# Kernel optimization log

Measured on AMD Instinct MI355X. Metric: run time of the kernel, lower is better.

Reference implementation:

```python
import jax, jax.numpy as jnp
import numpy as np

B = 4
S = 2_000_000
NPIX = 196608  # 12 * 128**2 (HEALPix nside=128)


def setup_inputs() -> dict:
    key = jax.random.key(0)
    k1, k2, k3, k4 = jax.random.split(key, 4)
    tod = jax.random.normal(k1, (B, S), dtype=jnp.float32)
    # per-sample Stokes weights (I, Q, U) of the pointing matrix rows
    weights = jax.random.normal(k2, (S, 3), dtype=jnp.float32)
    projection_cov = jax.random.uniform(k3, (NPIX,), dtype=jnp.float32)
    pix_idx = jax.random.randint(k4, (S,), 0, NPIX, dtype=jnp.int32)
    return {"tod": tod, "weights": weights, "projection_cov": projection_cov,
            "pix_idx": pix_idx}


def reference(tod, weights, projection_cov, pix_idx):
    npix = projection_cov.shape[0]
    # P^T: scatter-add each TOD sample's Stokes contribution into its pixel.
    # contrib: [B, S, 3]
    contrib = tod[:, :, None] * weights[None, :, :]
    sky = jax.vmap(
        lambda c: jax.ops.segment_sum(c, pix_idx, num_segments=npix)
    )(contrib)  # [B, npix, 3]
    # coverage normalization of I, Q, U
    sky = sky / projection_cov[None, :, None]
    return sky
```

## Files before the change

### kernel.cpp

```cpp
#include <hip/hip_runtime.h>


constexpr int NB   = 256;
constexpr int BW   = 768;
constexpr int NBLK = 256;
constexpr int TILE = 2048;
constexpr int RT   = 3072;


__device__ __forceinline__ unsigned f2bf(float f) {
    unsigned u = __float_as_uint(f);
    unsigned r = ((u >> 16) & 1u) + 0x7fffu;
    return (u + r) >> 16;
}
__device__ __forceinline__ float bf_lo(unsigned u) {
    return __uint_as_float(u << 16);
}
__device__ __forceinline__ float bf_hi(unsigned u) {
    return __uint_as_float(u & 0xffff0000u);
}


__global__ __launch_bounds__(1024)
void hist_kernel(const int* __restrict__ pix, int S, int chunk,
                 int* __restrict__ hist2d) {
    __shared__ int lh[NB];
    if (threadIdx.x < NB) lh[threadIdx.x] = 0;
    __syncthreads();
    const int beg = blockIdx.x * chunk;
    const int end = min(S, beg + chunk);
    for (int j = beg + threadIdx.x; j < end; j += blockDim.x)
        atomicAdd(&lh[pix[j] / BW], 1);
    __syncthreads();
    if (threadIdx.x < NB)
        hist2d[(size_t)blockIdx.x * NB + threadIdx.x] = lh[threadIdx.x];
}

__global__ __launch_bounds__(NBLK)
void scan_blocks_kernel(int* __restrict__ hist2d,
                        int* __restrict__ btotal) {
    __shared__ int sc[NBLK];
    const int bkt = blockIdx.x, tid = threadIdx.x;
    const int v = hist2d[(size_t)tid * NB + bkt];
    sc[tid] = v;
    __syncthreads();
    for (int off = 1; off < NBLK; off <<= 1) {
        int x = (tid >= off) ? sc[tid - off] : 0;
        __syncthreads();
        sc[tid] += x;
        __syncthreads();
    }
    hist2d[(size_t)tid * NB + bkt] = sc[tid] - v;
    if (tid == NBLK - 1) btotal[bkt] = sc[tid];
}

__global__ __launch_bounds__(NB)
void scan_buckets_kernel(const int* __restrict__ btotal,
                         int* __restrict__ bbase, int S) {
    __shared__ int sc[NB];
    const int tid = threadIdx.x;
    const int v = btotal[tid];
    sc[tid] = v;
    __syncthreads();
    for (int off = 1; off < NB; off <<= 1) {
        int x = (tid >= off) ? sc[tid - off] : 0;
        __syncthreads();
        sc[tid] += x;
        __syncthreads();
    }
    bbase[tid] = sc[tid] - v;
    if (tid == NB - 1) bbase[NB] = sc[tid];
}

__global__ __launch_bounds__(1024)
void reorder_sorted_kernel(const float* __restrict__ tod,
                           const float* __restrict__ weights,
                           const int* __restrict__ pix,
                           int S, int chunk,
                           const int* __restrict__ hist2d,
                           const int* __restrict__ bbase,
                           uint4* __restrict__ rec) {
    __shared__ unsigned       lrx[RT], lry[RT], lrz[RT], lrw[RT];
    __shared__ unsigned short lbk[RT];
    __shared__ unsigned short lidx[RT];
    __shared__ int            lbase[NB];
    __shared__ int            lcur[NB];
    __shared__ int            lstart[NB];

    const int blk = blockIdx.x;
    if (threadIdx.x < NB) {
        lbase[threadIdx.x] = bbase[threadIdx.x]
                           + hist2d[(size_t)blk * NB + threadIdx.x];
    }
    const int cbeg = blk * chunk;
    const int cend = min(S, cbeg + chunk);
    __syncthreads();

    for (int tbeg = cbeg; tbeg < cend; tbeg += RT) {
        const int n = min(RT, cend - tbeg);

        if (threadIdx.x < NB) lcur[threadIdx.x] = 0;
        __syncthreads();

        for (int jj = threadIdx.x; jj < n; jj += blockDim.x) {
            const int j = tbeg + jj;
            const int p = pix[j];
            const int bkt = p / BW;
            const int lp  = p - bkt * BW;
            const float w0 = weights[3 * j + 0];
            const float w1 = weights[3 * j + 1];
            const float w2 = weights[3 * j + 2];
            const float t0 = tod[(size_t)0 * S + j];
            const float t1 = tod[(size_t)1 * S + j];
            const float t2 = tod[(size_t)2 * S + j];
            const float t3 = tod[(size_t)3 * S + j];
            lrx[jj] = f2bf(w0) | (f2bf(w1) << 16);
            lry[jj] = f2bf(w2) | ((unsigned)lp << 16);
            lrz[jj] = f2bf(t0) | (f2bf(t1) << 16);
            lrw[jj] = f2bf(t2) | (f2bf(t3) << 16);
            lbk[jj] = (unsigned short)bkt;
            atomicAdd(&lcur[bkt], 1);
        }
        __syncthreads();

        if (threadIdx.x < 64) {
            const int i0 = threadIdx.x * 4;
            const int a0 = lcur[i0], a1 = lcur[i0 + 1];
            const int a2 = lcur[i0 + 2], a3 = lcur[i0 + 3];
            const int t1 = a0 + a1, t2 = t1 + a2, t3 = t2 + a3;
            int x = t3;
            #pragma unroll
            for (int off = 1; off < 64; off <<= 1) {
                const int y = __shfl_up(x, off, 64);
                if ((int)threadIdx.x >= off) x += y;
            }
            const int base = x - t3;
            lstart[i0]     = base;
            lstart[i0 + 1] = base + a0;
            lstart[i0 + 2] = base + t1;
            lstart[i0 + 3] = base + t2;
            lcur[i0]     = base;
            lcur[i0 + 1] = base + a0;
            lcur[i0 + 2] = base + t1;
            lcur[i0 + 3] = base + t2;
        }
        __syncthreads();

        for (int jj = threadIdx.x; jj < n; jj += blockDim.x) {
            const int r = atomicAdd(&lcur[lbk[jj]], 1);
            lidx[r] = (unsigned short)jj;
        }
        __syncthreads();

        for (int r = threadIdx.x; r < n; r += blockDim.x) {
            const int jj  = lidx[r];
            const int bkt = lbk[jj];
            uint4 v;
            v.x = lrx[jj]; v.y = lry[jj]; v.z = lrz[jj]; v.w = lrw[jj];
            rec[(size_t)(lbase[bkt] + (r - lstart[bkt]))] = v;
        }
        __syncthreads();

        if (threadIdx.x < NB)
            lbase[threadIdx.x] += lcur[threadIdx.x] - lstart[threadIdx.x];
        __syncthreads();
    }
}

__global__ __launch_bounds__(1024)
void accum_sort_kernel(const uint4* __restrict__ rec,
                       const float* __restrict__ cov,
                       const int* __restrict__ bbase,
                       float* __restrict__ out,
                       int npix) {
    __shared__ uint4          lrec[TILE];
    __shared__ unsigned short lpx[TILE];
    __shared__ unsigned short lidx[TILE];
    __shared__ int            start[BW + 1];
    __shared__ int            cur[BW];

    const int bkt = blockIdx.x;
    const int beg = bbase[bkt], end = bbase[bkt + 1];
    const int l = threadIdx.x & 255;
    const int q = threadIdx.x >> 8;
    float s00 = 0.f, s01 = 0.f, s02 = 0.f;
    float s10 = 0.f, s11 = 0.f, s12 = 0.f;
    float s20 = 0.f, s21 = 0.f, s22 = 0.f;

    for (int tbeg = beg; tbeg < end; tbeg += TILE) {
        const int n = min(TILE, end - tbeg);

        for (int t = threadIdx.x; t < BW; t += blockDim.x) cur[t] = 0;
        __syncthreads();
        for (int j = threadIdx.x; j < n; j += blockDim.x) {
            const uint4 r = rec[(size_t)(tbeg + j)];
            lrec[j] = r;
            const int lp = (int)(r.y >> 16);
            lpx[j] = (unsigned short)lp;
            atomicAdd(&cur[lp], 1);
        }
        __syncthreads();

        if (threadIdx.x < 64) {
            const int i0 = threadIdx.x * 12;
            int v[12], pre[12], run = 0;
            #pragma unroll
            for (int k = 0; k < 12; ++k) {
                v[k] = cur[i0 + k]; pre[k] = run; run += v[k];
            }
            int x = run;
            #pragma unroll
            for (int off = 1; off < 64; off <<= 1) {
                const int y = __shfl_up(x, off, 64);
                if ((int)threadIdx.x >= off) x += y;
            }
            const int base = x - run;
            #pragma unroll
            for (int k = 0; k < 12; ++k) {
                start[i0 + k] = base + pre[k];
                cur[i0 + k]   = base + pre[k];
            }
            if (threadIdx.x == 63) start[BW] = base + run;
        }
        __syncthreads();

        for (int j = threadIdx.x; j < n; j += blockDim.x) {
            const int r = atomicAdd(&cur[lpx[j]], 1);
            lidx[r] = (unsigned short)j;
        }
        __syncthreads();

        {
            const int rb = start[l], re = start[l + 1];
            for (int j = rb; j < re; ++j) {
                const int i = lidx[j];
                const uint4 r = lrec[i];
                const float tq = (q == 0) ? bf_lo(r.z) : (q == 1) ? bf_hi(r.z)
                               : (q == 2) ? bf_lo(r.w) : bf_hi(r.w);
                s00 += tq * bf_lo(r.x);
                s01 += tq * bf_hi(r.x);
                s02 += tq * bf_lo(r.y);
            }
        }
        {
            const int rb = start[l + 256], re = start[l + 257];
            for (int j = rb; j < re; ++j) {
                const int i = lidx[j];
                const uint4 r = lrec[i];
                const float tq = (q == 0) ? bf_lo(r.z) : (q == 1) ? bf_hi(r.z)
                               : (q == 2) ? bf_lo(r.w) : bf_hi(r.w);
                s10 += tq * bf_lo(r.x);
                s11 += tq * bf_hi(r.x);
                s12 += tq * bf_lo(r.y);
            }
        }
        {
            const int rb = start[l + 512], re = start[l + 513];
            for (int j = rb; j < re; ++j) {
                const int i = lidx[j];
                const uint4 r = lrec[i];
                const float tq = (q == 0) ? bf_lo(r.z) : (q == 1) ? bf_hi(r.z)
                               : (q == 2) ? bf_lo(r.w) : bf_hi(r.w);
                s20 += tq * bf_lo(r.x);
                s21 += tq * bf_hi(r.x);
                s22 += tq * bf_lo(r.y);
            }
        }
        __syncthreads();
    }

    {
        const int p = bkt * BW + l;
        const float rc = 1.0f / cov[p];
        const size_t o = ((size_t)q * npix + p) * 3;
        out[o + 0] = s00 * rc; out[o + 1] = s01 * rc; out[o + 2] = s02 * rc;
    }
    {
        const int p = bkt * BW + 256 + l;
        const float rc = 1.0f / cov[p];
        const size_t o = ((size_t)q * npix + p) * 3;
        out[o + 0] = s10 * rc; out[o + 1] = s11 * rc; out[o + 2] = s12 * rc;
    }
    {
        const int p = bkt * BW + 512 + l;
        const float rc = 1.0f / cov[p];
        const size_t o = ((size_t)q * npix + p) * 3;
        out[o + 0] = s20 * rc; out[o + 1] = s21 * rc; out[o + 2] = s22 * rc;
    }
}


__global__ void zero_out_kernel(float4* __restrict__ out, int n4) {
    int i = blockIdx.x * blockDim.x + threadIdx.x;
    int stride = gridDim.x * blockDim.x;
    for (; i < n4; i += stride) out[i] = make_float4(0.f, 0.f, 0.f, 0.f);
}

__global__ void scatter_kernel(const float* __restrict__ tod,
                               const float* __restrict__ weights,
                               const int*   __restrict__ pix,
                               float* __restrict__ out,
                               int S, int npix, int B) {
    int i = blockIdx.x * blockDim.x + threadIdx.x;
    int stride = gridDim.x * blockDim.x;
    const size_t bstride = (size_t)npix * 3;
    for (int s = i; s < S; s += stride) {
        const int p = pix[s];
        const float w0 = weights[3 * s + 0];
        const float w1 = weights[3 * s + 1];
        const float w2 = weights[3 * s + 2];
        float* o = out + (size_t)p * 3;
        for (int b = 0; b < B; ++b) {
            const float t = tod[(size_t)b * S + s];
            float* ob = o + (size_t)b * bstride;
            atomicAdd(ob + 0, t * w0);
            atomicAdd(ob + 1, t * w1);
            atomicAdd(ob + 2, t * w2);
        }
    }
}

__global__ void normalize_kernel(float* __restrict__ out,
                                 const float* __restrict__ cov,
                                 int npix, int B) {
    int i = blockIdx.x * blockDim.x + threadIdx.x;
    int stride = gridDim.x * blockDim.x;
    const int total = B * npix;
    for (; i < total; i += stride) {
        const int p = i % npix;
        const float c = cov[p];
        float* o = out + (size_t)i * 3;
        o[0] /= c; o[1] /= c; o[2] /= c;
    }
}


extern "C" void kernel_launch(void* const* d_in, const int* in_sizes, int n_in,
                              void* d_out, int out_size, void* d_ws, size_t ws_size,
                              hipStream_t stream) {
    const float* tod     = (const float*)d_in[0];
    const float* weights = (const float*)d_in[1];
    const float* cov     = (const float*)d_in[2];
    const int*   pix     = (const int*)d_in[3];
    float* out = (float*)d_out;

    const int S    = in_sizes[3];
    const int npix = in_sizes[2];
    const int B    = in_sizes[0] / S;

    const size_t meta_ints  = (size_t)NB * NBLK + NB + (NB + 1);
    const size_t meta_bytes = ((meta_ints * sizeof(int)) + 63) & ~(size_t)63;
    const size_t need_rec   = meta_bytes + (size_t)S * 16;

    const int chunk = (S + NBLK - 1) / NBLK;

    if (B == 4 && npix == NB * BW && ws_size >= need_rec) {
        int* hist2d = (int*)d_ws;
        int* btotal = hist2d + (size_t)NB * NBLK;
        int* bbase  = btotal + NB;
        uint4* rec  = (uint4*)((char*)d_ws + meta_bytes);

        hist_kernel<<<NBLK, 1024, 0, stream>>>(pix, S, chunk, hist2d);
        scan_blocks_kernel<<<NB, NBLK, 0, stream>>>(hist2d, btotal);
        scan_buckets_kernel<<<1, NB, 0, stream>>>(btotal, bbase, S);
        reorder_sorted_kernel<<<NBLK, 1024, 0, stream>>>(tod, weights, pix, S,
                                                         chunk, hist2d, bbase, rec);
        accum_sort_kernel<<<NB, 1024, 0, stream>>>(rec, cov, bbase, out, npix);
        return;
    }

    const int block = 256;
    {
        const int n4 = out_size / 4;
        int grid = min((n4 + block - 1) / block, 2048);
        zero_out_kernel<<<grid, block, 0, stream>>>((float4*)out, n4);
    }
    {
        int grid = min((S + block - 1) / block, 4096);
        scatter_kernel<<<grid, block, 0, stream>>>(tod, weights, pix, out, S, npix, B);
    }
    {
        const int total = B * npix;
        int grid = min((total + block - 1) / block, 2048);
        normalize_kernel<<<grid, block, 0, stream>>>(out, cov, npix, B);
    }
}
```

Baseline: 71.08 us.

## Split per-bucket accumulation across two blocks and add a reduce-normalize pass

Each pixel bucket's record range is now split into PARTS=2 halves, each handled by its own block, so the accumulation grid doubles from 256 to 512 blocks to fill more compute units. Each block writes unnormalized partial sums to a workspace buffer, and a new kernel adds the partials and applies the coverage normalization. The shared record tile also moves from uint4 to four separate unsigned arrays (structure-of-arrays) to change the LDS access pattern. In exchange it adds a kernel launch and extra global traffic to write and reread the partial sums, and it needs a larger workspace.

```diff
diff --git a/kernel.cpp b/kernel.cpp
--- a/kernel.cpp
+++ b/kernel.cpp
@@ -1,11 +1,12 @@
 #include <hip/hip_runtime.h>
 
 
-constexpr int NB   = 256;
-constexpr int BW   = 768;
-constexpr int NBLK = 256;
-constexpr int TILE = 2048;
-constexpr int RT   = 3072;
+constexpr int NB    = 256;
+constexpr int BW    = 768;
+constexpr int NBLK  = 256;
+constexpr int TILE  = 2048;
+constexpr int RT    = 3072;
+constexpr int PARTS = 2;
 
 
 __device__ __forceinline__ unsigned f2bf(float f) {
@@ -168,19 +169,24 @@
 }
 
 __global__ __launch_bounds__(1024)
-void accum_sort_kernel(const uint4* __restrict__ rec,
-                       const float* __restrict__ cov,
+void accum_part_kernel(const uint4* __restrict__ rec,
                        const int* __restrict__ bbase,
-                       float* __restrict__ out,
+                       float* __restrict__ partial,
                        int npix) {
-    __shared__ uint4          lrec[TILE];
+    __shared__ unsigned       lrx[TILE], lry[TILE], lrz[TILE], lrw[TILE];
     __shared__ unsigned short lpx[TILE];
     __shared__ unsigned short lidx[TILE];
     __shared__ int            start[BW + 1];
     __shared__ int            cur[BW];
 
-    const int bkt = blockIdx.x;
-    const int beg = bbase[bkt], end = bbase[bkt + 1];
+    const int bkt  = blockIdx.x / PARTS;
+    const int part = blockIdx.x - bkt * PARTS;
+    const int bbeg = bbase[bkt], bend = bbase[bkt + 1];
+    const int len  = bend - bbeg;
+    const int cl   = (len + PARTS - 1) / PARTS;
+    const int beg  = bbeg + part * cl;
+    const int end  = min(bend, beg + cl);
+
     const int l = threadIdx.x & 255;
     const int q = threadIdx.x >> 8;
     float s00 = 0.f, s01 = 0.f, s02 = 0.f;
@@ -194,7 +200,7 @@
         __syncthreads();
         for (int j = threadIdx.x; j < n; j += blockDim.x) {
             const uint4 r = rec[(size_t)(tbeg + j)];
-            lrec[j] = r;
+            lrx[j] = r.x; lry[j] = r.y; lrz[j] = r.z; lrw[j] = r.w;
             const int lp = (int)(r.y >> 16);
             lpx[j] = (unsigned short)lp;
             atomicAdd(&cur[lp], 1);
@@ -234,58 +240,79 @@
             const int rb = start[l], re = start[l + 1];
             for (int j = rb; j < re; ++j) {
                 const int i = lidx[j];
-                const uint4 r = lrec[i];
-                const float tq = (q == 0) ? bf_lo(r.z) : (q == 1) ? bf_hi(r.z)
-                               : (q == 2) ? bf_lo(r.w) : bf_hi(r.w);
-                s00 += tq * bf_lo(r.x);
-                s01 += tq * bf_hi(r.x);
-                s02 += tq * bf_lo(r.y);
+                const float tq = (q == 0) ? bf_lo(lrz[i]) : (q == 1) ? bf_hi(lrz[i])
+                               : (q == 2) ? bf_lo(lrw[i]) : bf_hi(lrw[i]);
+                s00 += tq * bf_lo(lrx[i]);
+                s01 += tq * bf_hi(lrx[i]);
+                s02 += tq * bf_lo(lry[i]);
             }
         }
         {
             const int rb = start[l + 256], re = start[l + 257];
             for (int j = rb; j < re; ++j) {
                 const int i = lidx[j];
-                const uint4 r = lrec[i];
-                const float tq = (q == 0) ? bf_lo(r.z) : (q == 1) ? bf_hi(r.z)
-                               : (q == 2) ? bf_lo(r.w) : bf_hi(r.w);
-                s10 += tq * bf_lo(r.x);
-                s11 += tq * bf_hi(r.x);
-                s12 += tq * bf_lo(r.y);
+                const float tq = (q == 0) ? bf_lo(lrz[i]) : (q == 1) ? bf_hi(lrz[i])
+                               : (q == 2) ? bf_lo(lrw[i]) : bf_hi(lrw[i]);
+                s10 += tq * bf_lo(lrx[i]);
+                s11 += tq * bf_hi(lrx[i]);
+                s12 += tq * bf_lo(lry[i]);
             }
         }
         {
             const int rb = start[l + 512], re = start[l + 513];
             for (int j = rb; j < re; ++j) {
                 const int i = lidx[j];
-                const uint4 r = lrec[i];
-                const float tq = (q == 0) ? bf_lo(r.z) : (q == 1) ? bf_hi(r.z)
-                               : (q == 2) ? bf_lo(r.w) : bf_hi(r.w);
-                s20 += tq * bf_lo(r.x);
-                s21 += tq * bf_hi(r.x);
-                s22 += tq * bf_lo(r.y);
-            }
-        }
-        __syncthreads();
-    }
-
+                const float tq = (q == 0) ? bf_lo(lrz[i]) : (q == 1) ? bf_hi(lrz[i])
+                               : (q == 2) ? bf_lo(lrw[i]) : bf_hi(lrw[i]);
+                s20 += tq * bf_lo(lrx[i]);
+                s21 += tq * bf_hi(lrx[i]);
+                s22 += tq * bf_lo(lry[i]);
+            }
+        }
+        __syncthreads();
+    }
+
+    const size_t plane = (size_t)4 * npix * 3;
     {
         const int p = bkt * BW + l;
+        const size_t o = part * plane + ((size_t)q * npix + p) * 3;
+        partial[o + 0] = s00; partial[o + 1] = s01; partial[o + 2] = s02;
+    }
+    {
+        const int p = bkt * BW + 256 + l;
+        const size_t o = part * plane + ((size_t)q * npix + p) * 3;
+        partial[o + 0] = s10; partial[o + 1] = s11; partial[o + 2] = s12;
+    }
+    {
+        const int p = bkt * BW + 512 + l;
+        const size_t o = part * plane + ((size_t)q * npix + p) * 3;
+        partial[o + 0] = s20; partial[o + 1] = s21; partial[o + 2] = s22;
+    }
+}
+
+__global__ __launch_bounds__(1024)
+void reduce_norm_kernel(const float* __restrict__ partial,
+                        const float* __restrict__ cov,
+                        float* __restrict__ out, int npix) {
+    const int total = 4 * npix;
+    const size_t plane = (size_t)4 * npix * 3;
+    int idx = blockIdx.x * blockDim.x + threadIdx.x;
+    const int stride = gridDim.x * blockDim.x;
+    for (; idx < total; idx += stride) {
+        const int q = idx / npix;
+        const int p = idx - q * npix;
         const float rc = 1.0f / cov[p];
         const size_t o = ((size_t)q * npix + p) * 3;
-        out[o + 0] = s00 * rc; out[o + 1] = s01 * rc; out[o + 2] = s02 * rc;
-    }
-    {
-        const int p = bkt * BW + 256 + l;
-        const float rc = 1.0f / cov[p];
-        const size_t o = ((size_t)q * npix + p) * 3;
-        out[o + 0] = s10 * rc; out[o + 1] = s11 * rc; out[o + 2] = s12 * rc;
-    }
-    {
-        const int p = bkt * BW + 512 + l;
-        const float rc = 1.0f / cov[p];
-        const size_t o = ((size_t)q * npix + p) * 3;
-        out[o + 0] = s20 * rc; out[o + 1] = s21 * rc; out[o + 2] = s22 * rc;
+        float a0 = partial[o + 0], a1 = partial[o + 1], a2 = partial[o + 2];
+        #pragma unroll
+        for (int pr = 1; pr < PARTS; ++pr) {
+            a0 += partial[pr * plane + o + 0];
+            a1 += partial[pr * plane + o + 1];
+            a2 += partial[pr * plane + o + 2];
+        }
+        out[o + 0] = a0 * rc;
+        out[o + 1] = a1 * rc;
+        out[o + 2] = a2 * rc;
     }
 }
 
@@ -350,7 +377,9 @@
 
     const size_t meta_ints  = (size_t)NB * NBLK + NB + (NB + 1);
     const size_t meta_bytes = ((meta_ints * sizeof(int)) + 63) & ~(size_t)63;
-    const size_t need_rec   = meta_bytes + (size_t)S * 16;
+    const size_t rec_bytes  = (size_t)S * 16;
+    const size_t part_bytes = (size_t)PARTS * 4 * npix * 3 * sizeof(float);
+    const size_t need_rec   = meta_bytes + rec_bytes + part_bytes;
 
     const int chunk = (S + NBLK - 1) / NBLK;
 
@@ -359,13 +388,19 @@
         int* btotal = hist2d + (size_t)NB * NBLK;
         int* bbase  = btotal + NB;
         uint4* rec  = (uint4*)((char*)d_ws + meta_bytes);
+        float* partial = (float*)((char*)d_ws + meta_bytes + rec_bytes);
 
         hist_kernel<<<NBLK, 1024, 0, stream>>>(pix, S, chunk, hist2d);
         scan_blocks_kernel<<<NB, NBLK, 0, stream>>>(hist2d, btotal);
         scan_buckets_kernel<<<1, NB, 0, stream>>>(btotal, bbase, S);
         reorder_sorted_kernel<<<NBLK, 1024, 0, stream>>>(tod, weights, pix, S,
                                                          chunk, hist2d, bbase, rec);
-        accum_sort_kernel<<<NB, 1024, 0, stream>>>(rec, cov, bbase, out, npix);
+        accum_part_kernel<<<NB * PARTS, 1024, 0, stream>>>(rec, bbase, partial, npix);
+        {
+            const int total = 4 * npix;
+            const int grid = (total + 1023) / 1024;
+            reduce_norm_kernel<<<grid, 1024, 0, stream>>>(partial, cov, out, npix);
+        }
         return;
     }
 
```

Result: faster. 69.65 us (-2.0%).
